# Kernel tuning notes

Measured on AMD Instinct MI355X. Metric: run time of the kernel, lower is better.

Reference implementation:

```python
import jax, jax.numpy as jnp
import numpy as np

EPS_SQRT = 1e-9
EPS_NORM = 1e-12


def setup_inputs() -> dict:
    key = jax.random.key(0)
    k1, k2 = jax.random.split(key)
    shape = (32, 112, 112, 128)  # B, H, W, C
    left = jax.random.normal(k1, shape, dtype=jnp.float32)
    right = jax.random.normal(k2, shape, dtype=jnp.float32)
    return {"left": left, "right": right}


def reference(left, right):
    B, H, W, C = left.shape
    # reshape to [B, H*W, C] and contract over the spatial dim -> [B, C, C]
    l = left.reshape(B, H * W, C)
    r = right.reshape(B, H * W, C)
    dotted = jnp.einsum('bxc,bxd->bcd', l, r)  # batched outer-product pooling
    flat = dotted.reshape(B, C * C)
    # signed square root
    sqrted = jnp.sign(flat) * jnp.sqrt(jnp.abs(flat) + EPS_SQRT)
    # L2 normalize over the flattened bilinear vector (tf.math.l2_normalize)
    sumsq = jnp.sum(jnp.square(sqrted), axis=-1, keepdims=True)
    normed = sqrted * jax.lax.rsqrt(jnp.maximum(sumsq, EPS_NORM))
    return normed
```

## Files before the change

kernel.cpp:

```cpp
#include <hip/hip_runtime.h>
#include <hip/hip_bf16.h>


#define NK      16
#define KC      784
#define BK      16
#define NT      49
#define BATCH   32
#define CDIM    128
#define XDIM    12544

typedef __bf16 bf16x8 __attribute__((ext_vector_type(8)));
typedef float  f32x16 __attribute__((ext_vector_type(16)));

__device__ float g_part[(size_t)NK * BATCH * CDIM * CDIM];
__device__ float g_ssq[BATCH * 16];

__device__ __forceinline__ void split4(const float* f, uint2& hi, uint2& lo) {
  uint xh[4], xl[4];
#pragma unroll
  for (int i = 0; i < 4; ++i) {
    uint u = __float_as_uint(f[i]);
    uint r = u + 0x7FFFu + ((u >> 16) & 1u);
    xh[i] = r;
    float hif = __uint_as_float(r & 0xFFFF0000u);
    xl[i] = __float_as_uint(f[i] - hif);
  }
  hi.x = __builtin_amdgcn_perm(xh[1], xh[0], 0x07060302u);
  hi.y = __builtin_amdgcn_perm(xh[3], xh[2], 0x07060302u);
  lo.x = __builtin_amdgcn_perm(xl[1], xl[0], 0x07060302u);
  lo.y = __builtin_amdgcn_perm(xl[3], xl[2], 0x07060302u);
}

__device__ __forceinline__ int ldsu(int c, int kh) {
  return ((c << 1) | kh) ^ ((c >> 2) & 7);
}

__global__ __launch_bounds__(512, 4)
void bcnn_gemm_kernel(const float* __restrict__ L, const float* __restrict__ R) {
  __shared__ uint2 sAhi[2][512], sAlo[2][512], sBhi[2][512], sBlo[2][512];

  const int chunk = blockIdx.x;
  const int b     = blockIdx.y;
  const int t     = threadIdx.x;
  const int l     = t & 63;
  const int w     = t >> 6;
  const int wr    = w >> 2;
  const int wc    = w & 3;
  const int lc    = l & 31;
  const int hh    = l >> 5;

  const int sc = t & 127;
  const int sh = t >> 7;
  const int wslot = ldsu(sc, sh >> 1) * 2 + (sh & 1);

  const float* gL = L + ((size_t)b * XDIM + (size_t)chunk * KC + sh * 4) * CDIM + sc;
  const float* gR = R + ((size_t)b * XDIM + (size_t)chunk * KC + sh * 4) * CDIM + sc;

  const int cA0 = wr * 64 + lc;
  const int cA1 = cA0 + 32;
  const int dB  = wc * 32 + lc;
  const int uA0 = ldsu(cA0, hh) * 2;
  const int uA1 = ldsu(cA1, hh) * 2;
  const int uB  = ldsu(dB,  hh) * 2;

  f32x16 acc0 = {};
  f32x16 acc1 = {};

  float rlE[4], rrE[4], rlO[4], rrO[4];

#define LOADR(rl, rr, s)                                                       \
  do {                                                                         \
    const float* pL_ = gL + (size_t)(s) * BK * CDIM;                           \
    const float* pR_ = gR + (size_t)(s) * BK * CDIM;                           \
    _Pragma("unroll")                                                          \
    for (int i = 0; i < 4; ++i) { rl[i] = pL_[i * CDIM]; rr[i] = pR_[i * CDIM]; } \
  } while (0)

#define WRITE(rl, rr, set)                                                     \
  do {                                                                         \
    uint2 hi_, lo_;                                                            \
    split4(rl, hi_, lo_);                                                      \
    sAhi[set][wslot] = hi_; sAlo[set][wslot] = lo_;                            \
    split4(rr, hi_, lo_);                                                      \
    sBhi[set][wslot] = hi_; sBlo[set][wslot] = lo_;                            \
  } while (0)

#define COMPUTE(set)                                                           \
  do {                                                                         \
    bf16x8 ah0 = *(const bf16x8*)&sAhi[set][uA0];                              \
    bf16x8 al0 = *(const bf16x8*)&sAlo[set][uA0];                              \
    bf16x8 ah1 = *(const bf16x8*)&sAhi[set][uA1];                              \
    bf16x8 al1 = *(const bf16x8*)&sAlo[set][uA1];                              \
    bf16x8 bh  = *(const bf16x8*)&sBhi[set][uB];                               \
    bf16x8 bl  = *(const bf16x8*)&sBlo[set][uB];                               \
    acc0 = __builtin_amdgcn_mfma_f32_32x32x16_bf16(ah0, bh, acc0, 0, 0, 0);    \
    acc1 = __builtin_amdgcn_mfma_f32_32x32x16_bf16(ah1, bh, acc1, 0, 0, 0);    \
    acc0 = __builtin_amdgcn_mfma_f32_32x32x16_bf16(ah0, bl, acc0, 0, 0, 0);    \
    acc1 = __builtin_amdgcn_mfma_f32_32x32x16_bf16(ah1, bl, acc1, 0, 0, 0);    \
    acc0 = __builtin_amdgcn_mfma_f32_32x32x16_bf16(al0, bh, acc0, 0, 0, 0);    \
    acc1 = __builtin_amdgcn_mfma_f32_32x32x16_bf16(al1, bh, acc1, 0, 0, 0);    \
  } while (0)

#define BAR()                                                                  \
  do {                                                                         \
    asm volatile("s_waitcnt lgkmcnt(0)" ::: "memory");                         \
    __builtin_amdgcn_s_barrier();                                              \
  } while (0)

  LOADR(rlE, rrE, 0);
  LOADR(rlO, rrO, 1);
  WRITE(rlE, rrE, 0);
  BAR();

  for (int it = 0; it < 24; ++it) {
    const int s0 = 2 * it;
    LOADR(rlE, rrE, s0 + 2);
    COMPUTE(0);
    WRITE(rlO, rrO, 1);
    BAR();
    if (s0 + 3 < NT) LOADR(rlO, rrO, s0 + 3);
    COMPUTE(1);
    WRITE(rlE, rrE, 0);
    BAR();
  }
  COMPUTE(0);

#undef LOADR
#undef WRITE
#undef COMPUTE
#undef BAR

  float* outp = g_part + (((size_t)chunk * BATCH + b) << 14);
#pragma unroll
  for (int r = 0; r < 16; ++r) {
    const int row = (r & 3) + ((r >> 2) << 3) + (hh << 2);
    outp[(size_t)(wr * 64 + row) * CDIM + (wc * 32 + lc)]      = acc0[r];
    outp[(size_t)(wr * 64 + 32 + row) * CDIM + (wc * 32 + lc)] = acc1[r];
  }
}

__global__ void bcnn_sqrt_kernel(float* __restrict__ out) {
  const int b   = blockIdx.y;
  const int seg = blockIdx.x;
  const int t   = threadIdx.x;
  const int idx = seg * 1024 + t * 4;

  float4 v = {0.f, 0.f, 0.f, 0.f};
#pragma unroll
  for (int ch = 0; ch < NK; ++ch) {
    const float4 p = *(const float4*)&g_part[(((size_t)ch * BATCH + b) << 14) + idx];
    v.x += p.x; v.y += p.y; v.z += p.z; v.w += p.w;
  }
  float4 sv;
  {
    float a;
    a = sqrtf(fabsf(v.x) + 1e-9f); sv.x = (v.x > 0.f) ? a : ((v.x < 0.f) ? -a : 0.f);
    a = sqrtf(fabsf(v.y) + 1e-9f); sv.y = (v.y > 0.f) ? a : ((v.y < 0.f) ? -a : 0.f);
    a = sqrtf(fabsf(v.z) + 1e-9f); sv.z = (v.z > 0.f) ? a : ((v.z < 0.f) ? -a : 0.f);
    a = sqrtf(fabsf(v.w) + 1e-9f); sv.w = (v.w > 0.f) ? a : ((v.w < 0.f) ? -a : 0.f);
  }
  *(float4*)&out[((size_t)b << 14) + idx] = sv;

  float ss = sv.x * sv.x + sv.y * sv.y + sv.z * sv.z + sv.w * sv.w;
#pragma unroll
  for (int o = 32; o > 0; o >>= 1) ss += __shfl_down(ss, o, 64);
  __shared__ float red[4];
  if ((t & 63) == 0) red[t >> 6] = ss;
  __syncthreads();
  if (t == 0) g_ssq[b * 16 + seg] = red[0] + red[1] + red[2] + red[3];
}

__global__ void bcnn_scale_kernel(float* __restrict__ out) {
  const int b   = blockIdx.y;
  const int seg = blockIdx.x;
  const int t   = threadIdx.x;

  float tot = 0.f;
#pragma unroll
  for (int i = 0; i < 16; ++i) tot += g_ssq[b * 16 + i];
  const float scale = rsqrtf(fmaxf(tot, 1e-12f));

  const size_t base = ((size_t)b << 14) + seg * 1024 + t * 4;
  float4 v = *(float4*)&out[base];
  v.x *= scale; v.y *= scale; v.z *= scale; v.w *= scale;
  *(float4*)&out[base] = v;
}

extern "C" void kernel_launch(void* const* d_in, const int* in_sizes, int n_in,
                              void* d_out, int out_size, void* d_ws, size_t ws_size,
                              hipStream_t stream) {
  const float* L = (const float*)d_in[0];
  const float* R = (const float*)d_in[1];
  float* out = (float*)d_out;

  dim3 g1(NK, BATCH);
  bcnn_gemm_kernel<<<g1, 512, 0, stream>>>(L, R);

  dim3 g2(16, BATCH);
  bcnn_sqrt_kernel<<<g2, 256, 0, stream>>>(out);
  bcnn_scale_kernel<<<g2, 256, 0, stream>>>(out);
}
```

Before: 96.18 us.

## Halve split-K chunks and double K-step per stage with wider LDS writes

Reduces the split-K factor from 16 to 8 chunks, so each block covers twice as many spatial rows and the partial-sum buffer and the reduction read in the sqrt kernel shrink by half. Each pipeline stage now loads 32 rows instead of 16, split into hi/lo bf16 as uint4 writes, and runs two MFMA sub-steps per barrier, halving the number of barriers per row. The grid drops to 256 blocks with launch bounds lowered to 2 blocks per CU, and registers per thread roughly double, which risks lower occupancy and less latency hiding. The loop count of 24 and NT of 49 are left unchanged, so the main loop covers 49*32 = 1568 rows per chunk, which matches the new KC.

```diff
diff --git a/kernel.cpp b/kernel.cpp
--- a/kernel.cpp
+++ b/kernel.cpp
@@ -2,9 +2,9 @@
 #include <hip/hip_bf16.h>
 
 
-#define NK      16
-#define KC      784
-#define BK      16
+#define NK      8
+#define KC      1568
+#define BK      32
 #define NT      49
 #define BATCH   32
 #define CDIM    128
@@ -16,10 +16,10 @@
 __device__ float g_part[(size_t)NK * BATCH * CDIM * CDIM];
 __device__ float g_ssq[BATCH * 16];
 
-__device__ __forceinline__ void split4(const float* f, uint2& hi, uint2& lo) {
-  uint xh[4], xl[4];
-#pragma unroll
-  for (int i = 0; i < 4; ++i) {
+__device__ __forceinline__ void split8(const float* f, uint4& hi, uint4& lo) {
+  uint xh[8], xl[8];
+#pragma unroll
+  for (int i = 0; i < 8; ++i) {
     uint u = __float_as_uint(f[i]);
     uint r = u + 0x7FFFu + ((u >> 16) & 1u);
     xh[i] = r;
@@ -28,17 +28,22 @@
   }
   hi.x = __builtin_amdgcn_perm(xh[1], xh[0], 0x07060302u);
   hi.y = __builtin_amdgcn_perm(xh[3], xh[2], 0x07060302u);
+  hi.z = __builtin_amdgcn_perm(xh[5], xh[4], 0x07060302u);
+  hi.w = __builtin_amdgcn_perm(xh[7], xh[6], 0x07060302u);
   lo.x = __builtin_amdgcn_perm(xl[1], xl[0], 0x07060302u);
   lo.y = __builtin_amdgcn_perm(xl[3], xl[2], 0x07060302u);
+  lo.z = __builtin_amdgcn_perm(xl[5], xl[4], 0x07060302u);
+  lo.w = __builtin_amdgcn_perm(xl[7], xl[6], 0x07060302u);
 }
 
 __device__ __forceinline__ int ldsu(int c, int kh) {
   return ((c << 1) | kh) ^ ((c >> 2) & 7);
 }
 
-__global__ __launch_bounds__(512, 4)
+__global__ __launch_bounds__(512, 2)
 void bcnn_gemm_kernel(const float* __restrict__ L, const float* __restrict__ R) {
-  __shared__ uint2 sAhi[2][512], sAlo[2][512], sBhi[2][512], sBlo[2][512];
+  __shared__ uint4 sAhi[2][2][256], sAlo[2][2][256];
+  __shared__ uint4 sBhi[2][2][256], sBlo[2][2][256];
 
   const int chunk = blockIdx.x;
   const int b     = blockIdx.y;
@@ -50,62 +55,66 @@
   const int lc    = l & 31;
   const int hh    = l >> 5;
 
-  const int sc = t & 127;
-  const int sh = t >> 7;
-  const int wslot = ldsu(sc, sh >> 1) * 2 + (sh & 1);
-
-  const float* gL = L + ((size_t)b * XDIM + (size_t)chunk * KC + sh * 4) * CDIM + sc;
-  const float* gR = R + ((size_t)b * XDIM + (size_t)chunk * KC + sh * 4) * CDIM + sc;
+  const int sc  = t & 127;
+  const int sh  = t >> 7;
+  const int sub = sh >> 1;
+  const int wu  = ldsu(sc, sh & 1);
+
+  const float* gL = L + ((size_t)b * XDIM + (size_t)chunk * KC + sh * 8) * CDIM + sc;
+  const float* gR = R + ((size_t)b * XDIM + (size_t)chunk * KC + sh * 8) * CDIM + sc;
 
   const int cA0 = wr * 64 + lc;
   const int cA1 = cA0 + 32;
   const int dB  = wc * 32 + lc;
-  const int uA0 = ldsu(cA0, hh) * 2;
-  const int uA1 = ldsu(cA1, hh) * 2;
-  const int uB  = ldsu(dB,  hh) * 2;
+  const int uA0 = ldsu(cA0, hh);
+  const int uA1 = ldsu(cA1, hh);
+  const int uB  = ldsu(dB,  hh);
 
   f32x16 acc0 = {};
   f32x16 acc1 = {};
 
-  float rlE[4], rrE[4], rlO[4], rrO[4];
-
-#define LOADR(rl, rr, s)                                                       \
-  do {                                                                         \
-    const float* pL_ = gL + (size_t)(s) * BK * CDIM;                           \
-    const float* pR_ = gR + (size_t)(s) * BK * CDIM;                           \
-    _Pragma("unroll")                                                          \
-    for (int i = 0; i < 4; ++i) { rl[i] = pL_[i * CDIM]; rr[i] = pR_[i * CDIM]; } \
-  } while (0)
-
-#define WRITE(rl, rr, set)                                                     \
-  do {                                                                         \
-    uint2 hi_, lo_;                                                            \
-    split4(rl, hi_, lo_);                                                      \
-    sAhi[set][wslot] = hi_; sAlo[set][wslot] = lo_;                            \
-    split4(rr, hi_, lo_);                                                      \
-    sBhi[set][wslot] = hi_; sBlo[set][wslot] = lo_;                            \
-  } while (0)
-
-#define COMPUTE(set)                                                           \
-  do {                                                                         \
-    bf16x8 ah0 = *(const bf16x8*)&sAhi[set][uA0];                              \
-    bf16x8 al0 = *(const bf16x8*)&sAlo[set][uA0];                              \
-    bf16x8 ah1 = *(const bf16x8*)&sAhi[set][uA1];                              \
-    bf16x8 al1 = *(const bf16x8*)&sAlo[set][uA1];                              \
-    bf16x8 bh  = *(const bf16x8*)&sBhi[set][uB];                               \
-    bf16x8 bl  = *(const bf16x8*)&sBlo[set][uB];                               \
-    acc0 = __builtin_amdgcn_mfma_f32_32x32x16_bf16(ah0, bh, acc0, 0, 0, 0);    \
-    acc1 = __builtin_amdgcn_mfma_f32_32x32x16_bf16(ah1, bh, acc1, 0, 0, 0);    \
-    acc0 = __builtin_amdgcn_mfma_f32_32x32x16_bf16(ah0, bl, acc0, 0, 0, 0);    \
-    acc1 = __builtin_amdgcn_mfma_f32_32x32x16_bf16(ah1, bl, acc1, 0, 0, 0);    \
-    acc0 = __builtin_amdgcn_mfma_f32_32x32x16_bf16(al0, bh, acc0, 0, 0, 0);    \
-    acc1 = __builtin_amdgcn_mfma_f32_32x32x16_bf16(al1, bh, acc1, 0, 0, 0);    \
-  } while (0)
-
-#define BAR()                                                                  \
-  do {                                                                         \
-    asm volatile("s_waitcnt lgkmcnt(0)" ::: "memory");                         \
-    __builtin_amdgcn_s_barrier();                                              \
+  float rlE[8], rrE[8], rlO[8], rrO[8];
+
+#define LOADR(rl, rr, s)                                                        \
+  do {                                                                          \
+    const float* pL_ = gL + (size_t)(s) * BK * CDIM;                            \
+    const float* pR_ = gR + (size_t)(s) * BK * CDIM;                            \
+    _Pragma("unroll")                                                           \
+    for (int i = 0; i < 8; ++i) { rl[i] = pL_[i * CDIM]; rr[i] = pR_[i * CDIM]; } \
+  } while (0)
+
+#define WRITE(rl, rr, set)                                                      \
+  do {                                                                          \
+    uint4 hi_, lo_;                                                             \
+    split8(rl, hi_, lo_);                                                       \
+    sAhi[set][sub][wu] = hi_; sAlo[set][sub][wu] = lo_;                         \
+    split8(rr, hi_, lo_);                                                       \
+    sBhi[set][sub][wu] = hi_; sBlo[set][sub][wu] = lo_;                         \
+  } while (0)
+
+#define COMPUTE(set)                                                            \
+  do {                                                                          \
+    _Pragma("unroll")                                                           \
+    for (int ss = 0; ss < 2; ++ss) {                                            \
+      bf16x8 ah0 = *(const bf16x8*)&sAhi[set][ss][uA0];                         \
+      bf16x8 al0 = *(const bf16x8*)&sAlo[set][ss][uA0];                         \
+      bf16x8 ah1 = *(const bf16x8*)&sAhi[set][ss][uA1];                         \
+      bf16x8 al1 = *(const bf16x8*)&sAlo[set][ss][uA1];                         \
+      bf16x8 bh  = *(const bf16x8*)&sBhi[set][ss][uB];                          \
+      bf16x8 bl  = *(const bf16x8*)&sBlo[set][ss][uB];                          \
+      acc0 = __builtin_amdgcn_mfma_f32_32x32x16_bf16(ah0, bh, acc0, 0, 0, 0);   \
+      acc1 = __builtin_amdgcn_mfma_f32_32x32x16_bf16(ah1, bh, acc1, 0, 0, 0);   \
+      acc0 = __builtin_amdgcn_mfma_f32_32x32x16_bf16(ah0, bl, acc0, 0, 0, 0);   \
+      acc1 = __builtin_amdgcn_mfma_f32_32x32x16_bf16(ah1, bl, acc1, 0, 0, 0);   \
+      acc0 = __builtin_amdgcn_mfma_f32_32x32x16_bf16(al0, bh, acc0, 0, 0, 0);   \
+      acc1 = __builtin_amdgcn_mfma_f32_32x32x16_bf16(al1, bh, acc1, 0, 0, 0);   \
+    }                                                                           \
+  } while (0)
+
+#define BAR()                                                                   \
+  do {                                                                          \
+    asm volatile("s_waitcnt lgkmcnt(0)" ::: "memory");                          \
+    __builtin_amdgcn_s_barrier();                                               \
   } while (0)
 
   LOADR(rlE, rrE, 0);
```

Measured after the change: 92.49 us. -3.8%, faster.
